# Kernel optimization log

Hardware: AMD Instinct MI355X
Metric: run time of the kernel (lower is better)

Reference implementation:

```python
import jax, jax.numpy as jnp
import numpy as np

N = 1024      # num_nodes
U = 64        # num_units
IN_DIM = 2    # input feature dim per node
B = 32        # batch
F = IN_DIM + U  # 66, input_size inside _gconv


def _xavier(k, shape):
    fan_in, fan_out = shape[-2], shape[-1]
    std = (2.0 / (fan_in + fan_out)) ** 0.5
    return jax.random.normal(k, shape, jnp.float32) * std


def setup_inputs() -> dict:
    key = jax.random.key(0)
    ks = jax.random.split(key, 14)
    return {
        "inputs": jax.random.normal(ks[0], (B, N * IN_DIM), jnp.float32),
        "hx": jax.random.normal(ks[1], (B, N * U), jnp.float32),
        "adj": jax.random.uniform(ks[2], (2, N, N), jnp.float32),
        "mask": jax.random.uniform(ks[3], (8, N, N), jnp.float32),
        # gate gconv params (output_size = 2U). Note: torch LayerParams caches by
        # shape, so weights_s/weights_i/weights_bp are ONE shared weight, ditto atts/atti.
        "W_ru": _xavier(ks[4], (F, 2 * U)),
        "Watt_ru": _xavier(ks[5], (N, 2 * U, 2 * U)),
        "Watt1_ru": _xavier(ks[6], (N, 2 * U, 1)),
        "Wout_ru": _xavier(ks[7], (6 * U, 2 * U)),
        "b_ru": jnp.ones((2 * U,), jnp.float32),   # bias_start=1.0
        # candidate gconv params (output_size = U)
        "W_c": _xavier(ks[8], (F, U)),
        "Watt_c": _xavier(ks[9], (N, U, U)),
        "Watt1_c": _xavier(ks[10], (N, U, 1)),
        "Wout_c": _xavier(ks[11], (3 * U, U)),
        "b_c": jnp.zeros((U,), jnp.float32),
    }


def _gconv(inputs, state, adj, mask, W, Watt, Watt1, Wout, b):
    Bs = inputs.shape[0]
    x = jnp.concatenate([inputs.reshape(Bs, N, -1), state.reshape(Bs, N, -1)], axis=2)  # [B,N,F]
    Ff = x.shape[2]
    x0 = x.transpose(1, 2, 0).reshape(N, Ff * Bs)  # [N, F*B]
    a0, a1 = adj[0], adj[1]
    # supports in the exact order of the torch loop:
    # adj0, mask0..3*adj0, mask4..7*adj1, adj1  -> 10 matrices
    mats = jnp.concatenate(
        [a0[None], mask[:4] * a0[None], mask[4:] * a1[None], a1[None]], axis=0
    )  # [10,N,N]
    xk = jnp.einsum('mij,jf->mif', mats, x0)  # [10,N,F*B]
    x_all = jnp.concatenate([x0[None], xk], axis=0).reshape(11, N, Ff, Bs)
    x_bp = x_all[0].transpose(2, 0, 1)        # [B,N,F]
    x_i = x_all[1:6].transpose(3, 1, 0, 2)    # [B,N,5,F]
    x_s = x_all[6:].transpose(3, 1, 0, 2)     # [B,N,5,F]
    x_i_p = x_i @ W        # [B,N,5,O] (shared weight, see LayerParams shape cache)
    x_s_p = x_s @ W        # [B,N,5,O]
    x_bp_p = x_bp @ W      # [B,N,O]

    def attend(xp):
        h = jax.nn.relu(jnp.einsum('bnko,noq->bnkq', xp, Watt))     # per-node weights
        s = jnp.einsum('bnkq,nqo->bnko', h, Watt1)[..., 0]          # [B,N,5]
        a = jax.nn.softmax(s, axis=-1)                              # over 5 supports
        return jnp.einsum('bnk,bnko->bno', a, xp)                   # [B,N,O]

    xi = attend(x_i_p)
    xs = attend(x_s_p)
    out = jnp.concatenate([xi, xs, x_bp_p], axis=-1) @ Wout + b     # [B,N,O]
    return out.reshape(Bs, -1)


def reference(inputs, hx, adj, mask, W_ru, Watt_ru, Watt1_ru, Wout_ru, b_ru,
              W_c, Watt_c, Watt1_c, Wout_c, b_c):
    value = jax.nn.sigmoid(_gconv(inputs, hx, adj, mask, W_ru, Watt_ru, Watt1_ru, Wout_ru, b_ru))
    value = value.reshape(-1, N, 2 * U)
    r = value[..., :U].reshape(-1, N * U)
    u = value[..., U:].reshape(-1, N * U)
    c = jnp.tanh(_gconv(inputs, r * hx, adj, mask, W_c, Watt_c, Watt1_c, Wout_c, b_c))
    return u * hx + (1.0 - u) * c
```

## Files before the change

kernel.cpp:

```cpp
#include <hip/hip_runtime.h>
#include <hip/hip_fp16.h>
#include <cstdint>
#include <cstddef>

#define NN 1024
#define BB 32

typedef _Float16 f16x8 __attribute__((ext_vector_type(8)));
typedef _Float16 f16x4 __attribute__((ext_vector_type(4)));
typedef float f32x4 __attribute__((ext_vector_type(4)));

__device__ __forceinline__ void load_lds16(const void* g, void* l) {
  __builtin_amdgcn_global_load_lds(
      (const __attribute__((address_space(1))) void*)g,
      (__attribute__((address_space(3))) void*)l, 16, 0, 0);
}

__device__ __forceinline__ void prep_body(
    int bid, int tid, const float* __restrict__ adj,
    const float* __restrict__ mask, _Float16* __restrict__ A,
    const float* __restrict__ Wru, const float* __restrict__ Wc,
    _Float16* __restrict__ WThru, _Float16* __restrict__ WTlru,
    _Float16* __restrict__ WThc, _Float16* __restrict__ WTlc) {
  if (bid < 1024) {
    int q = bid * 256 + tid;
    int i = q >> 8;
    int j0 = (q & 255) << 2;
    size_t off = (size_t)i * 1024 + j0;
    float4 a0 = *(const float4*)(adj + off);
    float4 a1 = *(const float4*)(adj + (1u << 20) + off);
    f16x4 r;
    r[0] = a0.x; r[1] = a0.y; r[2] = a0.z; r[3] = a0.w;
    *(f16x4*)(A + off) = r;
    r[0] = a1.x; r[1] = a1.y; r[2] = a1.z; r[3] = a1.w;
    *(f16x4*)(A + (size_t)9 * 1048576 + off) = r;
#pragma unroll
    for (int l = 0; l < 8; ++l) {
      float4 mk = *(const float4*)(mask + (size_t)l * 1048576 + off);
      float4 base = (l < 4) ? a0 : a1;
      r[0] = mk.x * base.x; r[1] = mk.y * base.y;
      r[2] = mk.z * base.z; r[3] = mk.w * base.w;
      *(f16x4*)(A + (size_t)(l + 1) * 1048576 + off) = r;
    }
  } else {
    int id = (bid - 1024) * 256 + tid;
    if (id < 128 * 384) {
      int o = id & 127, k = id >> 7;
      float w = Wru[k * 128 + o];
      _Float16 h = (_Float16)w;
      WThru[o * 384 + k] = h;
      WTlru[o * 384 + k] = (_Float16)(w - (float)h);
    } else {
      int id2 = id - 128 * 384;
      if (id2 < 64 * 192) {
        int o = id2 & 63, k = id2 >> 6;
        float w = Wc[k * 64 + o];
        _Float16 h = (_Float16)w;
        WThc[o * 192 + k] = h;
        WTlc[o * 192 + k] = (_Float16)(w - (float)h);
      }
    }
  }
}

template <int O>
__device__ __forceinline__ void proj0_body(
    int bx, const float* __restrict__ inp, const float* __restrict__ state,
    const float* __restrict__ W, _Float16* __restrict__ XP0,
    _Float16* __restrict__ XP0T) {
  constexpr int WR = O / 64;
  constexpr int WC = 4 / WR;
  constexpr int TN = WC * 64;
  constexpr int TPR = 256 / TN;
  __shared__ _Float16 ldsX[TN * 96];
  const int tid = threadIdx.x;
  const int c0 = bx * TN;
  const int b = c0 >> 10;
  const int l = tid & 63;
  const int w = tid >> 6;
  const int wr = w / WC, wc = w % WC;

  f16x8 af[4][3];
#pragma unroll
  for (int i = 0; i < 4; ++i) {
    int o = wr * 64 + i * 16 + (l & 15);
#pragma unroll
    for (int ks = 0; ks < 3; ++ks) {
#pragma unroll
      for (int e = 0; e < 8; ++e) {
        int f = ks * 32 + (l >> 4) * 8 + e;
        af[i][ks][e] = (f < 66) ? (_Float16)W[f * O + o] : (_Float16)0.f;
      }
    }
  }

  {
    const int row = (TPR == 2) ? (tid >> 1) : tid;
    const int h = (TPR == 2) ? (tid & 1) : 0;
    const int j = (c0 & 1023) + row;
    const float* sp = state + (size_t)b * 65536 + (size_t)j * 64;
    _Float16* ldsRow = ldsX + row * 96;
    const int rsw = row & 3;
    if (TPR == 1 || h == 0) {
      float2 in2 = *(const float2*)(inp + (size_t)b * 2048 + j * 2);
      float sv[48];
#pragma unroll
      for (int u = 0; u < 12; ++u)
        *(f32x4*)(sv + u * 4) = *(const f32x4*)(sp + u * 4);
      f16x8 v;
      v[0] = (_Float16)in2.x;
      v[1] = (_Float16)in2.y;
#pragma unroll
      for (int e = 2; e < 8; ++e) v[e] = (_Float16)sv[e - 2];
      *(f16x8*)(ldsRow + ((0 ^ rsw) << 3)) = v;
#pragma unroll
      for (int c = 1; c < 6; ++c) {
#pragma unroll
        for (int e = 0; e < 8; ++e) v[e] = (_Float16)sv[c * 8 + e - 2];
        int kt = c >> 2, cq = c & 3;
        *(f16x8*)(ldsRow + kt * 32 + ((cq ^ rsw) << 3)) = v;
      }
    }
    if (TPR == 1 || h == 1) {
      float sv2[20];
#pragma unroll
      for (int u = 0; u < 5; ++u)
        *(f32x4*)(sv2 + u * 4) = *(const f32x4*)(sp + 44 + u * 4);
      f16x8 v;
#pragma unroll
      for (int e = 0; e < 8; ++e) v[e] = (_Float16)sv2[2 + e];
      *(f16x8*)(ldsRow + 32 + ((2 ^ rsw) << 3)) = v;
#pragma unroll
      for (int e = 0; e < 8; ++e) v[e] = (_Float16)sv2[10 + e];
      *(f16x8*)(ldsRow + 32 + ((3 ^ rsw) << 3)) = v;
      v[0] = (_Float16)sv2[18];
      v[1] = (_Float16)sv2[19];
#pragma unroll
      for (int e = 2; e < 8; ++e) v[e] = (_Float16)0.f;
      *(f16x8*)(ldsRow + 64 + ((0 ^ rsw) << 3)) = v;
#pragma unroll
      for (int e = 0; e < 8; ++e) v[e] = (_Float16)0.f;
      *(f16x8*)(ldsRow + 64 + ((1 ^ rsw) << 3)) = v;
      *(f16x8*)(ldsRow + 64 + ((2 ^ rsw) << 3)) = v;
      *(f16x8*)(ldsRow + 64 + ((3 ^ rsw) << 3)) = v;
    }
  }
  __syncthreads();

  const int ps = ((l >> 4) ^ (l & 3)) * 8;
  int offB[4];
#pragma unroll
  for (int j = 0; j < 4; ++j)
    offB[j] = (wc * 64 + j * 16 + (l & 15)) * 96 + ps;

  f32x4 acc[4][4];
#pragma unroll
  for (int i = 0; i < 4; ++i)
#pragma unroll
    for (int j = 0; j < 4; ++j) acc[i][j] = (f32x4){0.f, 0.f, 0.f, 0.f};

#pragma unroll
  for (int kt = 0; kt < 3; ++kt) {
    f16x8 bf[4];
#pragma unroll
    for (int j = 0; j < 4; ++j)
      bf[j] = *(const f16x8*)(&ldsX[offB[j] + kt * 32]);
#pragma unroll
    for (int i = 0; i < 4; ++i)
#pragma unroll
      for (int j = 0; j < 4; ++j)
        acc[i][j] = __builtin_amdgcn_mfma_f32_16x16x32_f16(af[i][kt], bf[j],
                                                           acc[i][j], 0, 0, 0);
  }

#pragma unroll
  for (int i = 0; i < 4; ++i) {
    int ob = wr * 64 + i * 16 + (l >> 4) * 4;
#pragma unroll
    for (int j = 0; j < 4; ++j) {
      int jn = (c0 & 1023) + wc * 64 + j * 16 + (l & 15);
      f16x4 hv;
#pragma unroll
      for (int r = 0; r < 4; ++r) {
        hv[r] = (_Float16)acc[i][j][r];
        XP0T[((size_t)b * O + ob + r) * 1024 + jn] = hv[r];
      }
      *(f16x4*)(XP0 + ((size_t)jn * 32 + b) * O + ob) = hv;
    }
  }
}

__global__ __launch_bounds__(256, 2) void k_front(
    const float* __restrict__ inputs, const float* __restrict__ hx,
    const float* __restrict__ W_ru, _Float16* __restrict__ XP0,
    _Float16* __restrict__ XP0T, const float* __restrict__ adj,
    const float* __restrict__ mask, _Float16* __restrict__ A,
    const float* __restrict__ Wru, const float* __restrict__ Wc,
    _Float16* __restrict__ WThru, _Float16* __restrict__ WTlru,
    _Float16* __restrict__ WThc, _Float16* __restrict__ WTlc) {
  if (blockIdx.x < 256) {
    proj0_body<128>(blockIdx.x, inputs, hx, W_ru, XP0, XP0T);
  } else {
    prep_body(blockIdx.x - 256, threadIdx.x, adj, mask, A, Wru, Wc, WThru,
              WTlru, WThc, WTlc);
  }
}

__global__ __launch_bounds__(256, 2) void k_proj0_c(
    const float* __restrict__ inp, const float* __restrict__ state,
    const float* __restrict__ W, _Float16* __restrict__ XP0,
    _Float16* __restrict__ XP0T) {
  proj0_body<64>(blockIdx.x, inp, state, W, XP0, XP0T);
}

template <int CN>
__global__ __launch_bounds__(256, 2) void k_supports2_mfma(
    const _Float16* __restrict__ A, const _Float16* __restrict__ BT,
    _Float16* __restrict__ XPD) {
  __shared__ _Float16 ldsU[4][4096];
  const int tid = threadIdx.x;
  const int bn = blockIdx.x;
  const int bm = blockIdx.y;
  const int l = tid & 63;
  const int w = tid >> 6;
  const int wr = w >> 1, wc = w & 1;

  const int t0 = tid, t1 = 256 + tid;
  const int r0 = t0 >> 2, q0 = (t0 & 3) ^ (r0 & 3);
  const int r1 = t1 >> 2, q1 = (t1 & 3) ^ (r1 & 3);
  const _Float16* gA0 = A + ((size_t)(bm * 128 + r0)) * 1024 + q0 * 8;
  const _Float16* gA1 = A + ((size_t)(bm * 128 + r1)) * 1024 + q1 * 8;
  const _Float16* gB0 = BT + ((size_t)(bn * 128 + r0)) * 1024 + q0 * 8;
  const _Float16* gB1 = BT + ((size_t)(bn * 128 + r1)) * 1024 + q1 * 8;

  const int ps = ((l >> 4) ^ (l & 3)) * 8;
  int offA[4], offB[4];
#pragma unroll
  for (int i = 0; i < 4; ++i) {
    offA[i] = (wr * 64 + i * 16 + (l & 15)) * 32 + ps;
    offB[i] = (wc * 64 + i * 16 + (l & 15)) * 32 + ps;
  }

  f32x4 acc[4][4];
#pragma unroll
  for (int i = 0; i < 4; ++i)
#pragma unroll
    for (int j = 0; j < 4; ++j) acc[i][j] = (f32x4){0.f, 0.f, 0.f, 0.f};

  load_lds16(gA0, &ldsU[0][0] + t0 * 8);
  load_lds16(gA1, &ldsU[0][0] + t1 * 8);
  load_lds16(gB0, &ldsU[2][0] + t0 * 8);
  load_lds16(gB1, &ldsU[2][0] + t1 * 8);

  int buf = 0;
  for (int kt = 0; kt < 32; ++kt) {
    __syncthreads();
    if (kt + 1 < 32) {
      int k0 = (kt + 1) * 32;
      load_lds16(gA0 + k0, &ldsU[buf ^ 1][0] + t0 * 8);
      load_lds16(gA1 + k0, &ldsU[buf ^ 1][0] + t1 * 8);
      load_lds16(gB0 + k0, &ldsU[2 + (buf ^ 1)][0] + t0 * 8);
      load_lds16(gB1 + k0, &ldsU[2 + (buf ^ 1)][0] + t1 * 8);
    }
    f16x8 af[4], bf[4];
#pragma unroll
    for (int i = 0; i < 4; ++i)
      af[i] = *(const f16x8*)(&ldsU[buf][offA[i]]);
#pragma unroll
    for (int i = 0; i < 4; ++i)
      bf[i] = *(const f16x8*)(&ldsU[2 + buf][offB[i]]);
#pragma unroll
    for (int i = 0; i < 4; ++i)
#pragma unroll
      for (int j = 0; j < 4; ++j)
        acc[i][j] = __builtin_amdgcn_mfma_f32_16x16x32_f16(af[i], bf[j],
                                                           acc[i][j], 0, 0, 0);
    buf ^= 1;
  }

  __syncthreads();
  {
    _Float16* C = &ldsU[0][0];
#pragma unroll
    for (int i = 0; i < 4; ++i) {
      int Rl = wr * 64 + i * 16 + (l >> 4) * 4;
#pragma unroll
      for (int j = 0; j < 4; ++j) {
        int Cc = wc * 64 + j * 16 + (l & 15);
#pragma unroll
        for (int r = 0; r < 4; ++r) {
          int row = Rl + r;
          C[row * 128 + (((Cc >> 3) ^ (row & 7)) << 3) + (Cc & 7)] =
              (_Float16)acc[i][j][r];
        }
      }
    }
    __syncthreads();
#pragma unroll
    for (int it = 0; it < 8; ++it) {
      int flat = it * 256 + tid;
      int row = flat >> 4;
      int c2 = flat & 15;
      f16x8 v = *(const f16x8*)(&C[row * 128 + ((c2 ^ (row & 7)) << 3)]);
      *(f16x8*)(XPD + (size_t)(bm * 128 + row) * CN + bn * 128 + c2 * 8) = v;
    }
  }
}

template <int O>
__global__ __launch_bounds__(256) void k_attend_mfma(
    const __half* __restrict__ XPD, const float* __restrict__ Watt,
    const float* __restrict__ Watt1, _Float16* __restrict__ CAT2h,
    _Float16* __restrict__ CAT2l) {
  constexpr int MTW = O / 64;
  constexpr int KS = O / 32;
  constexpr int SLOTS = O / 8;
  constexpr int SWZ = SLOTS - 1;
  const int n = blockIdx.x;
  const int tid = threadIdx.x;
  const int l = tid & 63;
  const int w = tid >> 6;

  __shared__ _Float16 xpL[160 * O];
  __shared__ float sPartL[4][160];
  __shared__ float aL[32][5];

  const int qbase = w * (O / 4);
  f16x8 afr[MTW][KS];
#pragma unroll
  for (int mt = 0; mt < MTW; ++mt) {
    const int q = qbase + mt * 16 + (l & 15);
#pragma unroll
    for (int ks = 0; ks < KS; ++ks) {
#pragma unroll
      for (int e = 0; e < 8; ++e) {
        int o = ks * 32 + (l >> 4) * 8 + e;
        afr[mt][ks][e] = (_Float16)Watt[((size_t)n * O + o) * O + q];
      }
    }
  }
  float wt1[MTW][4];
#pragma unroll
  for (int mt = 0; mt < MTW; ++mt)
#pragma unroll
    for (int r = 0; r < 4; ++r)
      wt1[mt][r] = Watt1[(size_t)n * O + qbase + mt * 16 + (l >> 4) * 4 + r];

  for (int g = 0; g < 2; ++g) {
    if (g) __syncthreads();
    {
      const f16x8* xsrc = reinterpret_cast<const f16x8*>(XPD);
      f16x8* xdst = reinterpret_cast<f16x8*>(xpL);
      for (int p = tid; p < 160 * SLOTS; p += 256) {
        int row = p / SLOTS;
        int sc = p - row * SLOTS;
        int phys = sc ^ (row & SWZ);
        int si = row >> 5, b = row & 31;
        size_t gi = ((size_t)(g * 5 + si) * 1024 + n) * (size_t)(4 * O) +
                    b * (O / 8) + sc;
        xdst[row * SLOTS + phys] = xsrc[gi];
      }
    }
    __syncthreads();

    for (int nt = 0; nt < 10; ++nt) {
      f32x4 acc[MTW];
#pragma unroll
      for (int mt = 0; mt < MTW; ++mt) acc[mt] = (f32x4){0.f, 0.f, 0.f, 0.f};
      const int row = nt * 16 + (l & 15);
#pragma unroll
      for (int ks = 0; ks < KS; ++ks) {
        int phys = (ks * 4 + (l >> 4)) ^ (row & SWZ);
        f16x8 bf = *(const f16x8*)(&xpL[row * O + phys * 8]);
#pragma unroll
        for (int mt = 0; mt < MTW; ++mt)
          acc[mt] = __builtin_amdgcn_mfma_f32_16x16x32_f16(afr[mt][ks], bf,
                                                           acc[mt], 0, 0, 0);
      }
      float sp = 0.f;
#pragma unroll
      for (int mt = 0; mt < MTW; ++mt)
#pragma unroll
        for (int r = 0; r < 4; ++r)
          sp += fmaxf(acc[mt][r], 0.f) * wt1[mt][r];
      sp += __shfl_xor(sp, 16);
      sp += __shfl_xor(sp, 32);
      if (l < 16) sPartL[w][nt * 16 + l] = sp;
    }
    __syncthreads();

    if (tid < 32) {
      const int b = tid;
      float sv[5];
#pragma unroll
      for (int k = 0; k < 5; ++k) {
        int row = k * 32 + b;
        sv[k] = sPartL[0][row] + sPartL[1][row] + sPartL[2][row] +
                sPartL[3][row];
      }
      float mx = sv[0];
#pragma unroll
      for (int k = 1; k < 5; ++k) mx = fmaxf(mx, sv[k]);
      float e[5], sum = 0.f;
#pragma unroll
      for (int k = 0; k < 5; ++k) {
        e[k] = expf(sv[k] - mx);
        sum += e[k];
      }
      float inv = 1.f / sum;
#pragma unroll
      for (int k = 0; k < 5; ++k) aL[b][k] = e[k] * inv;
    }
    __syncthreads();

    for (int it = 0; it < SLOTS * 32 / 256; ++it) {
      int idx = it * 256 + tid;
      int b = idx & 31;
      int sc = idx >> 5;
      float o8[8] = {0.f, 0.f, 0.f, 0.f, 0.f, 0.f, 0.f, 0.f};
#pragma unroll
      for (int si = 0; si < 5; ++si) {
        int row = si * 32 + b;
        int phys = sc ^ (row & SWZ);
        f16x8 xv = *(const f16x8*)(&xpL[row * O + phys * 8]);
        float a = aL[b][si];
#pragma unroll
        for (int j = 0; j < 8; ++j) o8[j] += a * (float)xv[j];
      }
      f16x8 hv, lv;
#pragma unroll
      for (int j = 0; j < 8; ++j) {
        hv[j] = (_Float16)o8[j];
        lv[j] = (_Float16)(o8[j] - (float)hv[j]);
      }
      size_t doff = ((size_t)n * 32 + b) * (2 * O) + g * O + sc * 8;
      *reinterpret_cast<f16x8*>(CAT2h + doff) = hv;
      *reinterpret_cast<f16x8*>(CAT2l + doff) = lv;
    }
  }
}

__global__ __launch_bounds__(256, 2) void k_wout_ru_mfma(
    const _Float16* __restrict__ CAT2h, const _Float16* __restrict__ CAT2l,
    const _Float16* __restrict__ XP0, const _Float16* __restrict__ WTh,
    const _Float16* __restrict__ WTl, const float* __restrict__ bias,
    const float* __restrict__ hx, float* __restrict__ RHX,
    float* __restrict__ UBUF) {
  constexpr int KTOT = 384, KC = 8, KT = 12;
  __shared__ _Float16 ldsAh[2][4096];
  __shared__ _Float16 ldsAl[2][4096];
  __shared__ _Float16 ldsBh[2][4096];
  __shared__ _Float16 ldsBl[2][4096];
  const int tid = threadIdx.x;
  const int blk = blockIdx.x;
  const int l = tid & 63;
  const int w = tid >> 6;
  const int wr = w >> 1, wc = w & 1;

  const int t0 = tid, t1 = 256 + tid;
  const int r0 = t0 >> 2, q0 = (t0 & 3) ^ (r0 & 3);
  const int r1 = t1 >> 2, q1 = (t1 & 3) ^ (r1 & 3);
  const size_t R0 = (size_t)blk * 128 + r0, R1 = (size_t)blk * 128 + r1;
  const _Float16* pA0ch = CAT2h + R0 * 256 + q0 * 8;
  const _Float16* pA1ch = CAT2h + R1 * 256 + q1 * 8;
  const _Float16* pA0cl = CAT2l + R0 * 256 + q0 * 8;
  const _Float16* pA1cl = CAT2l + R1 * 256 + q1 * 8;
  const _Float16* pA0x = XP0 + R0 * 128 + q0 * 8;
  const _Float16* pA1x = XP0 + R1 * 128 + q1 * 8;
  const _Float16* pB0h = WTh + (size_t)r0 * KTOT + q0 * 8;
  const _Float16* pB1h = WTh + (size_t)r1 * KTOT + q1 * 8;
  const _Float16* pB0l = WTl + (size_t)r0 * KTOT + q0 * 8;
  const _Float16* pB1l = WTl + (size_t)r1 * KTOT + q1 * 8;

  const int ps = ((l >> 4) ^ (l & 3)) * 8;
  int offA[4], offB[4];
#pragma unroll
  for (int i = 0; i < 4; ++i) {
    offA[i] = (wr * 64 + i * 16 + (l & 15)) * 32 + ps;
    offB[i] = (wc * 64 + i * 16 + (l & 15)) * 32 + ps;
  }

  f32x4 acc[4][4];
#pragma unroll
  for (int i = 0; i < 4; ++i)
#pragma unroll
    for (int j = 0; j < 4; ++j) acc[i][j] = (f32x4){0.f, 0.f, 0.f, 0.f};

  load_lds16(pA0ch, &ldsAh[0][0] + t0 * 8);
  load_lds16(pA1ch, &ldsAh[0][0] + t1 * 8);
  load_lds16(pA0cl, &ldsAl[0][0] + t0 * 8);
  load_lds16(pA1cl, &ldsAl[0][0] + t1 * 8);
  load_lds16(pB0h, &ldsBh[0][0] + t0 * 8);
  load_lds16(pB1h, &ldsBh[0][0] + t1 * 8);
  load_lds16(pB0l, &ldsBl[0][0] + t0 * 8);
  load_lds16(pB1l, &ldsBl[0][0] + t1 * 8);

  int buf = 0;
  for (int kt = 0; kt < KT; ++kt) {
    __syncthreads();
    if (kt + 1 < KT) {
      int k1 = kt + 1;
      const _Float16* a0 =
          (k1 < KC) ? pA0ch + k1 * 32 : pA0x + (k1 - KC) * 32;
      const _Float16* a1 =
          (k1 < KC) ? pA1ch + k1 * 32 : pA1x + (k1 - KC) * 32;
      load_lds16(a0, &ldsAh[buf ^ 1][0] + t0 * 8);
      load_lds16(a1, &ldsAh[buf ^ 1][0] + t1 * 8);
      if (k1 < KC) {
        load_lds16(pA0cl + k1 * 32, &ldsAl[buf ^ 1][0] + t0 * 8);
        load_lds16(pA1cl + k1 * 32, &ldsAl[buf ^ 1][0] + t1 * 8);
      }
      load_lds16(pB0h + k1 * 32, &ldsBh[buf ^ 1][0] + t0 * 8);
      load_lds16(pB1h + k1 * 32, &ldsBh[buf ^ 1][0] + t1 * 8);
      load_lds16(pB0l + k1 * 32, &ldsBl[buf ^ 1][0] + t0 * 8);
      load_lds16(pB1l + k1 * 32, &ldsBl[buf ^ 1][0] + t1 * 8);
    }
    f16x8 ah[4], bh[4], bl[4];
#pragma unroll
    for (int i = 0; i < 4; ++i) ah[i] = *(const f16x8*)(&ldsAh[buf][offA[i]]);
#pragma unroll
    for (int i = 0; i < 4; ++i) bh[i] = *(const f16x8*)(&ldsBh[buf][offB[i]]);
#pragma unroll
    for (int i = 0; i < 4; ++i) bl[i] = *(const f16x8*)(&ldsBl[buf][offB[i]]);
#pragma unroll
    for (int i = 0; i < 4; ++i)
#pragma unroll
      for (int j = 0; j < 4; ++j) {
        acc[i][j] = __builtin_amdgcn_mfma_f32_16x16x32_f16(ah[i], bh[j],
                                                           acc[i][j], 0, 0, 0);
        acc[i][j] = __builtin_amdgcn_mfma_f32_16x16x32_f16(ah[i], bl[j],
                                                           acc[i][j], 0, 0, 0);
      }
    if (kt < KC) {
      f16x8 al[4];
#pragma unroll
      for (int i = 0; i < 4; ++i)
        al[i] = *(const f16x8*)(&ldsAl[buf][offA[i]]);
#pragma unroll
      for (int i = 0; i < 4; ++i)
#pragma unroll
        for (int j = 0; j < 4; ++j)
          acc[i][j] = __builtin_amdgcn_mfma_f32_16x16x32_f16(al[i], bh[j],
                                                             acc[i][j], 0, 0, 0);
    }
    buf ^= 1;
  }

#pragma unroll
  for (int i = 0; i < 4; ++i) {
    int R = blk * 128 + wr * 64 + i * 16 + (l >> 4) * 4;
#pragma unroll
    for (int j = 0; j < 4; ++j) {
      int o = wc * 64 + j * 16 + (l & 15);
      float bv = bias[o];
#pragma unroll
      for (int rr = 0; rr < 4; ++rr) {
        int Rr = R + rr;
        int n = Rr >> 5, b = Rr & 31;
        size_t base = ((size_t)b * NN + n) * 64;
        float val = 1.f / (1.f + expf(-(acc[i][j][rr] + bv)));
        if (o < 64)
          RHX[base + o] = val * hx[base + o];
        else
          UBUF[base + (o - 64)] = val;
      }
    }
  }
}

__global__ __launch_bounds__(256, 2) void k_wout_c_mfma(
    const _Float16* __restrict__ CAT2h, const _Float16* __restrict__ XP0,
    const _Float16* __restrict__ WTh, const float* __restrict__ bias,
    const float* __restrict__ UBUF, const float* __restrict__ hx,
    float* __restrict__ out) {
  constexpr int KTOT = 192, KC = 4, KT = 6;
  __shared__ _Float16 ldsAh[2][4096];
  __shared__ _Float16 ldsBh[2][2048];
  const int tid = threadIdx.x;
  const int blk = blockIdx.x;
  const int l = tid & 63;
  const int w = tid >> 6;

  const int t0 = tid, t1 = 256 + tid;
  const int r0 = t0 >> 2, q0 = (t0 & 3) ^ (r0 & 3);
  const int r1 = t1 >> 2, q1 = (t1 & 3) ^ (r1 & 3);
  const size_t R0 = (size_t)blk * 128 + r0, R1 = (size_t)blk * 128 + r1;
  const _Float16* pA0ch = CAT2h + R0 * 128 + q0 * 8;
  const _Float16* pA1ch = CAT2h + R1 * 128 + q1 * 8;
  const _Float16* pA0x = XP0 + R0 * 64 + q0 * 8;
  const _Float16* pA1x = XP0 + R1 * 64 + q1 * 8;
  const int rb = tid >> 2, qb = (tid & 3) ^ (rb & 3);
  const _Float16* pBh = WTh + (size_t)rb * KTOT + qb * 8;

  const int ps = ((l >> 4) ^ (l & 3)) * 8;
  int offA[2], offB[4];
#pragma unroll
  for (int i = 0; i < 2; ++i)
    offA[i] = (w * 32 + i * 16 + (l & 15)) * 32 + ps;
#pragma unroll
  for (int j = 0; j < 4; ++j) offB[j] = (j * 16 + (l & 15)) * 32 + ps;

  f32x4 acc[2][4];
#pragma unroll
  for (int i = 0; i < 2; ++i)
#pragma unroll
    for (int j = 0; j < 4; ++j) acc[i][j] = (f32x4){0.f, 0.f, 0.f, 0.f};

  load_lds16(pA0ch, &ldsAh[0][0] + t0 * 8);
  load_lds16(pA1ch, &ldsAh[0][0] + t1 * 8);
  load_lds16(pBh, &ldsBh[0][0] + tid * 8);

  int buf = 0;
  for (int kt = 0; kt < KT; ++kt) {
    __syncthreads();
    if (kt + 1 < KT) {
      int k1 = kt + 1;
      const _Float16* a0 =
          (k1 < KC) ? pA0ch + k1 * 32 : pA0x + (k1 - KC) * 32;
      const _Float16* a1 =
          (k1 < KC) ? pA1ch + k1 * 32 : pA1x + (k1 - KC) * 32;
      load_lds16(a0, &ldsAh[buf ^ 1][0] + t0 * 8);
      load_lds16(a1, &ldsAh[buf ^ 1][0] + t1 * 8);
      load_lds16(pBh + k1 * 32, &ldsBh[buf ^ 1][0] + tid * 8);
    }
    f16x8 ah[2], bh[4];
#pragma unroll
    for (int i = 0; i < 2; ++i) ah[i] = *(const f16x8*)(&ldsAh[buf][offA[i]]);
#pragma unroll
    for (int j = 0; j < 4; ++j) bh[j] = *(const f16x8*)(&ldsBh[buf][offB[j]]);
#pragma unroll
    for (int i = 0; i < 2; ++i)
#pragma unroll
      for (int j = 0; j < 4; ++j)
        acc[i][j] = __builtin_amdgcn_mfma_f32_16x16x32_f16(ah[i], bh[j],
                                                           acc[i][j], 0, 0, 0);
    buf ^= 1;
  }

#pragma unroll
  for (int i = 0; i < 2; ++i) {
    int R = blk * 128 + w * 32 + i * 16 + (l >> 4) * 4;
#pragma unroll
    for (int j = 0; j < 4; ++j) {
      int o = j * 16 + (l & 15);
      float bv = bias[o];
#pragma unroll
      for (int rr = 0; rr < 4; ++rr) {
        int Rr = R + rr;
        int n = Rr >> 5, b = Rr & 31;
        size_t idx = ((size_t)b * NN + n) * 64 + o;
        float cval = tanhf(acc[i][j][rr] + bv);
        float u = UBUF[idx];
        out[idx] = u * hx[idx] + (1.f - u) * cval;
      }
    }
  }
}

extern "C" void kernel_launch(void* const* d_in, const int* in_sizes, int n_in,
                              void* d_out, int out_size, void* d_ws,
                              size_t ws_size, hipStream_t stream) {
  const float* inputs   = (const float*)d_in[0];
  const float* hx       = (const float*)d_in[1];
  const float* adj      = (const float*)d_in[2];
  const float* mask     = (const float*)d_in[3];
  const float* W_ru     = (const float*)d_in[4];
  const float* Watt_ru  = (const float*)d_in[5];
  const float* Watt1_ru = (const float*)d_in[6];
  const float* Wout_ru  = (const float*)d_in[7];
  const float* b_ru     = (const float*)d_in[8];
  const float* W_c      = (const float*)d_in[9];
  const float* Watt_c   = (const float*)d_in[10];
  const float* Watt1_c  = (const float*)d_in[11];
  const float* Wout_c   = (const float*)d_in[12];
  const float* b_c      = (const float*)d_in[13];

  char* ws = (char*)d_ws;
  _Float16*  XPD   = (_Float16*)(ws + 6291456);
  _Float16*  XP0   = (_Float16*)(ws + 90177536);
  _Float16*  XP0T  = (_Float16*)(ws + 98566144);
  _Float16*  CAT2h = (_Float16*)(ws + 106954752);
  _Float16*  CAT2l = (_Float16*)(ws + 123731968);
  float*     RHX   = (float*)(ws + 140509184);
  float*     UBUF  = (float*)(ws + 148897792);
  _Float16*  A_all = (_Float16*)(ws + 157286400);
  _Float16*  WThru = (_Float16*)(ws + 178257920);
  _Float16*  WTlru = (_Float16*)(ws + 178356224);
  _Float16*  WThc  = (_Float16*)(ws + 178454528);
  _Float16*  WTlc  = (_Float16*)(ws + 178479104);
  float*     out   = (float*)d_out;

  k_front<<<1520, 256, 0, stream>>>(inputs, hx, W_ru, XP0, XP0T, adj, mask,
                                    A_all, Wout_ru, Wout_c, WThru, WTlru,
                                    WThc, WTlc);
  k_supports2_mfma<4096><<<dim3(32, 80), 256, 0, stream>>>(A_all, XP0T, XPD);
  k_attend_mfma<128><<<1024, 256, 0, stream>>>((const __half*)XPD, Watt_ru,
                                               Watt1_ru, CAT2h, CAT2l);
  k_wout_ru_mfma<<<256, 256, 0, stream>>>(CAT2h, CAT2l, XP0, WThru, WTlru,
                                          b_ru, hx, RHX, UBUF);
  k_proj0_c<<<128, 256, 0, stream>>>(inputs, RHX, W_c, XP0, XP0T);
  k_supports2_mfma<2048><<<dim3(16, 80), 256, 0, stream>>>(A_all, XP0T, XPD);
  k_attend_mfma<64><<<1024, 256, 0, stream>>>((const __half*)XPD, Watt_c,
                                              Watt1_c, CAT2h, CAT2l);
  k_wout_c_mfma<<<256, 256, 0, stream>>>(CAT2h, XP0, WThc, b_c,
                                         UBUF, hx, out);
}
```

Measured before the change: 312.1 us.

## Triple-buffer LDS pipeline in supports GEMM with explicit vmcnt waits

Turns the double-buffered global-to-LDS load loop in the support-matrix MFMA GEMM into a three-stage ring buffer. Two tiles are prefetched ahead, and an explicit s_waitcnt vmcnt(4) replaces the implicit full drain before each barrier, so loads stay in flight longer. LDS use grows from 32KB to 48KB per block, which may limit how many blocks fit per CU.

```diff
diff --git a/kernel.cpp b/kernel.cpp
--- a/kernel.cpp
+++ b/kernel.cpp
@@ -217,7 +217,7 @@
 __global__ __launch_bounds__(256, 2) void k_supports2_mfma(
     const _Float16* __restrict__ A, const _Float16* __restrict__ BT,
     _Float16* __restrict__ XPD) {
-  __shared__ _Float16 ldsU[4][4096];
+  __shared__ _Float16 ldsU[6][4096];
   const int tid = threadIdx.x;
   const int bn = blockIdx.x;
   const int bm = blockIdx.y;
@@ -233,6 +233,15 @@
   const _Float16* gB0 = BT + ((size_t)(bn * 128 + r0)) * 1024 + q0 * 8;
   const _Float16* gB1 = BT + ((size_t)(bn * 128 + r1)) * 1024 + q1 * 8;
 
+#define STAGE_R3(t, s)                                   \
+  {                                                      \
+    int k0_ = (t) * 32;                                  \
+    load_lds16(gA0 + k0_, &ldsU[(s)][0] + t0 * 8);       \
+    load_lds16(gA1 + k0_, &ldsU[(s)][0] + t1 * 8);       \
+    load_lds16(gB0 + k0_, &ldsU[3 + (s)][0] + t0 * 8);   \
+    load_lds16(gB1 + k0_, &ldsU[3 + (s)][0] + t1 * 8);   \
+  }
+
   const int ps = ((l >> 4) ^ (l & 3)) * 8;
   int offA[4], offB[4];
 #pragma unroll
@@ -247,36 +256,36 @@
 #pragma unroll
     for (int j = 0; j < 4; ++j) acc[i][j] = (f32x4){0.f, 0.f, 0.f, 0.f};
 
-  load_lds16(gA0, &ldsU[0][0] + t0 * 8);
-  load_lds16(gA1, &ldsU[0][0] + t1 * 8);
-  load_lds16(gB0, &ldsU[2][0] + t0 * 8);
-  load_lds16(gB1, &ldsU[2][0] + t1 * 8);
-
-  int buf = 0;
+  STAGE_R3(0, 0);
+  STAGE_R3(1, 1);
+
+  int slot = 0;
   for (int kt = 0; kt < 32; ++kt) {
-    __syncthreads();
-    if (kt + 1 < 32) {
-      int k0 = (kt + 1) * 32;
-      load_lds16(gA0 + k0, &ldsU[buf ^ 1][0] + t0 * 8);
-      load_lds16(gA1 + k0, &ldsU[buf ^ 1][0] + t1 * 8);
-      load_lds16(gB0 + k0, &ldsU[2 + (buf ^ 1)][0] + t0 * 8);
-      load_lds16(gB1 + k0, &ldsU[2 + (buf ^ 1)][0] + t1 * 8);
-    }
+    if (kt < 31)
+      asm volatile("s_waitcnt vmcnt(4)" ::: "memory");
+    else
+      asm volatile("s_waitcnt vmcnt(0)" ::: "memory");
+    __builtin_amdgcn_sched_barrier(0);
+    __builtin_amdgcn_s_barrier();
+    __builtin_amdgcn_sched_barrier(0);
+    const int s2 = (slot >= 1) ? slot - 1 : 2;
+    if (kt + 2 < 32) STAGE_R3(kt + 2, s2);
     f16x8 af[4], bf[4];
 #pragma unroll
     for (int i = 0; i < 4; ++i)
-      af[i] = *(const f16x8*)(&ldsU[buf][offA[i]]);
+      af[i] = *(const f16x8*)(&ldsU[slot][offA[i]]);
 #pragma unroll
     for (int i = 0; i < 4; ++i)
-      bf[i] = *(const f16x8*)(&ldsU[2 + buf][offB[i]]);
+      bf[i] = *(const f16x8*)(&ldsU[3 + slot][offB[i]]);
 #pragma unroll
     for (int i = 0; i < 4; ++i)
 #pragma unroll
       for (int j = 0; j < 4; ++j)
         acc[i][j] = __builtin_amdgcn_mfma_f32_16x16x32_f16(af[i], bf[j],
                                                            acc[i][j], 0, 0, 0);
-    buf ^= 1;
-  }
+    slot = (slot == 2) ? 0 : slot + 1;
+  }
+#undef STAGE_R3
 
   __syncthreads();
   {
```

Measured after the change: 309.4 us. Within noise of the previous version (-0.9%).
